# Performance work log

Hardware: AMD Instinct MI355X
Metric: run time of the kernel (lower is better)

Reference implementation:

```python
import jax, jax.numpy as jnp
import numpy as np

B, S, D, H = 2, 2048, 1024, 16
DK = D // H  # 64


def setup_inputs() -> dict:
    key = jax.random.key(0)
    ks = jax.random.split(key, 9)
    s = 0.02
    return {
        "embeddings": jax.random.normal(ks[0], (B, S, D), jnp.float32),
        "Wq": jax.random.normal(ks[1], (H, D, DK), jnp.float32) * s,
        "bq": jax.random.normal(ks[2], (H, DK), jnp.float32) * s,
        "Wk": jax.random.normal(ks[3], (H, D, DK), jnp.float32) * s,
        "bk": jax.random.normal(ks[4], (H, DK), jnp.float32) * s,
        "Wv": jax.random.normal(ks[5], (H, D, DK), jnp.float32) * s,
        "bv": jax.random.normal(ks[6], (H, DK), jnp.float32) * s,
        "Wo": jax.random.normal(ks[7], (D, D), jnp.float32) * s,
        "bo": jax.random.normal(ks[8], (D,), jnp.float32) * s,
    }


def reference(embeddings, Wq, bq, Wk, bk, Wv, bv, Wo, bo):
    b, s, d = embeddings.shape
    dk = Wq.shape[-1]
    # batched per-head projections: [b,s,d] x [h,d,k] -> [b,h,s,k]
    q = jnp.einsum('bsd,hdk->bhsk', embeddings, Wq) + bq[None, :, None, :]
    k = jnp.einsum('bsd,hdk->bhsk', embeddings, Wk) + bk[None, :, None, :]
    v = jnp.einsum('bsd,hdk->bhsk', embeddings, Wv) + bv[None, :, None, :]
    scores = jnp.einsum('bhqk,bhsk->bhqs', q, k) / jnp.sqrt(jnp.float32(dk))
    causal_mask = jnp.triu(jnp.ones((s, s), dtype=bool), k=1)  # True above diagonal
    scores = jnp.where(causal_mask, jnp.float32(-1e9), scores)
    weights = jax.nn.softmax(scores, axis=-1)
    ctx = jnp.einsum('bhqs,bhsk->bhqk', weights, v)
    concat = ctx.transpose(0, 2, 1, 3).reshape(b, s, d)  # head-major concat, matches torch.cat
    return concat @ Wo + bo
```

## Files before the change

### kernel.cpp

```cpp
#include <hip/hip_runtime.h>
#include <hip/hip_bf16.h>

typedef unsigned short u16;
typedef unsigned int u32;
typedef __bf16 bf16x8 __attribute__((ext_vector_type(8)));
typedef float f32x4 __attribute__((ext_vector_type(4)));

#define AS1 __attribute__((address_space(1)))
#define AS3 __attribute__((address_space(3)))

#define NB 2
#define NS 2048
#define ND 1024
#define NH 16
#define NK 64

__device__ __forceinline__ u16 f2bf(float f) {
  u32 u = __builtin_bit_cast(u32, f);
  return (u16)((u + 0x7FFFu + ((u >> 16) & 1u)) >> 16);
}

__device__ __forceinline__ u32 cvt_pk_bf16(float lo, float hi) {
  u32 u;
  asm("v_cvt_pk_bf16_f32 %0, %1, %2" : "=v"(u) : "v"(lo), "v"(hi));
  return u;
}

__device__ __forceinline__ void stage_tile(u16* lds, const u16* __restrict__ src, int rs,
                                           int wid, int lane) {
#pragma unroll
  for (int i = 0; i < 2; ++i) {
    int c = wid * 128 + i * 64 + lane;
    int row = c >> 3;
    int kc = (c & 7) ^ (row & 7);
    __builtin_amdgcn_global_load_lds((const AS1 u32*)(src + row * rs + kc * 8),
                                     (AS3 u32*)(lds + (wid * 128 + i * 64) * 8), 16, 0, 0);
  }
}

__device__ __forceinline__ bf16x8 read_frag(const u16* lds, int row, int ks, int lane) {
  int slot = ((lane >> 4) + ks * 4) ^ (row & 7);
  return *(const bf16x8*)(lds + row * 64 + slot * 8);
}

__global__ __launch_bounds__(256) void convert_kernel(const float* __restrict__ src,
                                                      u16* __restrict__ dst, int n) {
  int i = (blockIdx.x * 256 + threadIdx.x) * 4;
  if (i >= n) return;
  float4 v = *(const float4*)(src + i);
  u32 w0 = cvt_pk_bf16(v.x, v.y);
  u32 w1 = cvt_pk_bf16(v.z, v.w);
  uint2 w; w.x = w0; w.y = w1;
  *(uint2*)(dst + i) = w;
}

__global__ __launch_bounds__(256) void transpose_conv(const float* __restrict__ src,
                                                      u16* __restrict__ dst, int R, int C) {
  __shared__ float tile[32][33];
  size_t base = (size_t)blockIdx.z * R * C;
  src += base;
  dst += base;
  int c0 = blockIdx.x * 32, r0 = blockIdx.y * 32;
  int tx = threadIdx.x, ty = threadIdx.y;
#pragma unroll
  for (int i = 0; i < 4; ++i)
    tile[ty + 8 * i][tx] = src[(size_t)(r0 + ty + 8 * i) * C + c0 + tx];
  __syncthreads();
#pragma unroll
  for (int i = 0; i < 4; ++i)
    dst[(size_t)(c0 + ty + 8 * i) * R + r0 + tx] = f2bf(tile[tx][ty + 8 * i]);
}

__global__ __launch_bounds__(256) void qkv_kernel(
    const u16* __restrict__ emb, const u16* __restrict__ Wqt, const u16* __restrict__ Wkt,
    const u16* __restrict__ Wvt, const float* __restrict__ bq, const float* __restrict__ bk,
    const float* __restrict__ bv, u16* __restrict__ Q, u16* __restrict__ K,
    u16* __restrict__ Vt) {
  __shared__ alignas(16) u16 lds_a[64 * 64];
  __shared__ alignas(16) u16 lds_b[64 * 64];
  int tid = threadIdx.x, lane = tid & 63, wid = tid >> 6;
  int mt = blockIdx.x, h = blockIdx.y, which = blockIdx.z;
  const u16* Wt = (which == 0 ? Wqt : which == 1 ? Wkt : Wvt) + h * (ND * NK);
  const float* bias = (which == 0 ? bq : which == 1 ? bk : bv) + h * NK;
  int m0 = mt * 64;
  int col = lane & 15;
  f32x4 zero4 = {0.f, 0.f, 0.f, 0.f};
  f32x4 acc[4] = {zero4, zero4, zero4, zero4};
  for (int k0 = 0; k0 < ND; k0 += 64) {
    stage_tile(lds_a, emb + m0 * ND + k0, ND, wid, lane);
    stage_tile(lds_b, Wt + k0, ND, wid, lane);
    __syncthreads();
#pragma unroll
    for (int ks = 0; ks < 2; ++ks) {
      bf16x8 a = read_frag(lds_a, wid * 16 + col, ks, lane);
#pragma unroll
      for (int f = 0; f < 4; ++f) {
        bf16x8 b = read_frag(lds_b, f * 16 + col, ks, lane);
        acc[f] = __builtin_amdgcn_mfma_f32_16x16x32_bf16(a, b, acc[f], 0, 0, 0);
      }
    }
    __syncthreads();
  }
  int rbase = m0 + wid * 16 + (lane >> 4) * 4;
#pragma unroll
  for (int f = 0; f < 4; ++f) {
    int n = f * 16 + col;
    float bn = bias[n];
#pragma unroll
    for (int r = 0; r < 4; ++r) {
      int m = rbase + r;
      int b = m >> 11, s = m & (NS - 1);
      float v = acc[f][r] + bn;
      if (which == 0) {
        Q[((b * NH + h) * NS + s) * NK + n] = f2bf(v * 0.18033688f);
      } else if (which == 1) {
        K[((b * NH + h) * NS + s) * NK + n] = f2bf(v);
      } else {
        Vt[((b * NH + h) * NK + n) * NS + s] = f2bf(v);
      }
    }
  }
}

__global__ __launch_bounds__(256) void attn_kernel(const u16* __restrict__ Q,
                                                   const u16* __restrict__ K,
                                                   const u16* __restrict__ Vt,
                                                   u16* __restrict__ ctx) {
  __shared__ alignas(16) u16 lds_k[2][64 * 64];
  __shared__ alignas(16) u16 lds_v[2][64 * 64];
  __shared__ alignas(16) u16 p_lds[4][16 * 72];
  int tid = threadIdx.x, lane = tid & 63, wid = tid >> 6;
  int bh = blockIdx.x;
  int pr = blockIdx.y;
  const u16* Qb = Q + bh * (NS * NK);
  const u16* Kb = K + bh * (NS * NK);
  const u16* Vb = Vt + bh * (NK * NS);
  int col = lane & 15;
  int b = bh >> 4, h = bh & 15;
  f32x4 zero4 = {0.f, 0.f, 0.f, 0.f};
  u16* pw = p_lds[wid];

#pragma unroll 1
  for (int half = 0; half < 2; ++half) {
    int qt = half ? pr : (31 - pr);
    int q0 = qt * 64;
    int qrow_a = q0 + wid * 16 + col;
    bf16x8 qf0 = *(const bf16x8*)(Qb + qrow_a * NK + (lane >> 4) * 8);
    bf16x8 qf1 = *(const bf16x8*)(Qb + qrow_a * NK + 32 + (lane >> 4) * 8);
    f32x4 acc[4] = {zero4, zero4, zero4, zero4};
    float m[4], lp[4];
#pragma unroll
    for (int r = 0; r < 4; ++r) { m[r] = -1e30f; lp[r] = 0.f; }
    int qrow_c = q0 + wid * 16 + (lane >> 4) * 4;
    int nt = qt + 1;

    stage_tile(lds_k[0], Kb, NK, wid, lane);
    stage_tile(lds_v[0], Vb, NS, wid, lane);
    __syncthreads();

    for (int t = 0; t < nt; ++t) {
      int cur = t & 1;
      if (t + 1 < nt) {
        stage_tile(lds_k[cur ^ 1], Kb + (t + 1) * 64 * NK, NK, wid, lane);
        stage_tile(lds_v[cur ^ 1], Vb + (t + 1) * 64, NS, wid, lane);
      }
      const u16* lk = lds_k[cur];
      const u16* lv = lds_v[cur];
      f32x4 sc[4];
#pragma unroll
      for (int f = 0; f < 4; ++f) {
        bf16x8 b0 = read_frag(lk, f * 16 + col, 0, lane);
        sc[f] = __builtin_amdgcn_mfma_f32_16x16x32_bf16(qf0, b0, zero4, 0, 0, 0);
        bf16x8 b1 = read_frag(lk, f * 16 + col, 1, lane);
        sc[f] = __builtin_amdgcn_mfma_f32_16x16x32_bf16(qf1, b1, sc[f], 0, 0, 0);
      }
      if (t == qt) {
#pragma unroll
        for (int f = 0; f < 4; ++f) {
          int kg = t * 64 + f * 16 + col;
#pragma unroll
          for (int r = 0; r < 4; ++r)
            if (kg > qrow_c + r) sc[f][r] = -1e30f;
        }
      }
      float mx[4];
#pragma unroll
      for (int r = 0; r < 4; ++r)
        mx[r] = fmaxf(fmaxf(sc[0][r], sc[1][r]), fmaxf(sc[2][r], sc[3][r]));
#pragma unroll
      for (int off = 1; off < 16; off <<= 1)
#pragma unroll
        for (int r = 0; r < 4; ++r) mx[r] = fmaxf(mx[r], __shfl_xor(mx[r], off));
      bool ok = true;
#pragma unroll
      for (int r = 0; r < 4; ++r) ok = ok && (mx[r] <= m[r] + 8.0f);
      if (!__all(ok)) {
#pragma unroll
        for (int r = 0; r < 4; ++r) {
          float mn = fmaxf(m[r], mx[r]);
          float al = exp2f(m[r] - mn);
          m[r] = mn;
          lp[r] *= al;
#pragma unroll
          for (int f = 0; f < 4; ++f) acc[f][r] *= al;
        }
      }
#pragma unroll
      for (int f = 0; f < 4; ++f)
#pragma unroll
        for (int r = 0; r < 4; ++r) {
          float p = exp2f(sc[f][r] - m[r]);
          sc[f][r] = p;
          lp[r] += p;
        }
#pragma unroll
      for (int f = 0; f < 4; ++f)
#pragma unroll
        for (int rp = 0; rp < 4; rp += 2) {
          u32 u = cvt_pk_bf16(sc[f][rp], sc[f][rp + 1]);
          int row = (lane >> 4) * 4 + rp;
          pw[row * 72 + f * 16 + col] = (u16)u;
          pw[(row + 1) * 72 + f * 16 + col] = (u16)(u >> 16);
        }
#pragma unroll
      for (int ks = 0; ks < 2; ++ks) {
        bf16x8 pa = *(const bf16x8*)(pw + col * 72 + ks * 32 + (lane >> 4) * 8);
#pragma unroll
        for (int f = 0; f < 4; ++f) {
          bf16x8 vb = read_frag(lv, f * 16 + col, ks, lane);
          acc[f] = __builtin_amdgcn_mfma_f32_16x16x32_bf16(pa, vb, acc[f], 0, 0, 0);
        }
      }
      __syncthreads();
    }
#pragma unroll
    for (int off = 1; off < 16; off <<= 1)
#pragma unroll
      for (int r = 0; r < 4; ++r) lp[r] += __shfl_xor(lp[r], off);
#pragma unroll
    for (int r = 0; r < 4; ++r) {
      float inv = 1.0f / lp[r];
      int s = qrow_c + r;
#pragma unroll
      for (int f = 0; f < 4; ++f)
        ctx[(b * NS + s) * ND + h * NK + f * 16 + col] = f2bf(acc[f][r] * inv);
    }
  }
}

__global__ __launch_bounds__(256) void outproj_kernel(const u16* __restrict__ ctx,
                                                      const u16* __restrict__ Wot,
                                                      const float* __restrict__ bo,
                                                      float* __restrict__ out) {
  __shared__ alignas(16) u16 lds_a[64 * 64];
  __shared__ alignas(16) u16 lds_b[64 * 64];
  int tid = threadIdx.x, lane = tid & 63, wid = tid >> 6;
  int m0 = blockIdx.x * 64, n0 = blockIdx.y * 64;
  int col = lane & 15;
  f32x4 zero4 = {0.f, 0.f, 0.f, 0.f};
  f32x4 acc[4] = {zero4, zero4, zero4, zero4};
  for (int k0 = 0; k0 < ND; k0 += 64) {
    stage_tile(lds_a, ctx + m0 * ND + k0, ND, wid, lane);
    stage_tile(lds_b, Wot + n0 * ND + k0, ND, wid, lane);
    __syncthreads();
#pragma unroll
    for (int ks = 0; ks < 2; ++ks) {
      bf16x8 a = read_frag(lds_a, wid * 16 + col, ks, lane);
#pragma unroll
      for (int f = 0; f < 4; ++f) {
        bf16x8 b = read_frag(lds_b, f * 16 + col, ks, lane);
        acc[f] = __builtin_amdgcn_mfma_f32_16x16x32_bf16(a, b, acc[f], 0, 0, 0);
      }
    }
    __syncthreads();
  }
  int rbase = m0 + wid * 16 + (lane >> 4) * 4;
#pragma unroll
  for (int f = 0; f < 4; ++f) {
    int n = n0 + f * 16 + col;
    float bn = bo[n];
#pragma unroll
    for (int r = 0; r < 4; ++r) out[(rbase + r) * ND + n] = acc[f][r] + bn;
  }
}

extern "C" void kernel_launch(void* const* d_in, const int* in_sizes, int n_in,
                              void* d_out, int out_size, void* d_ws, size_t ws_size,
                              hipStream_t stream) {
  (void)in_sizes; (void)n_in; (void)out_size;
  const float* emb = (const float*)d_in[0];
  const float* Wq = (const float*)d_in[1];
  const float* bq = (const float*)d_in[2];
  const float* Wk = (const float*)d_in[3];
  const float* bk = (const float*)d_in[4];
  const float* Wv = (const float*)d_in[5];
  const float* bv = (const float*)d_in[6];
  const float* Wo = (const float*)d_in[7];
  const float* bo = (const float*)d_in[8];
  float* out = (float*)d_out;

  const size_t EMB_N = (size_t)NB * NS * ND;
  const size_t W_N = (size_t)NH * ND * NK;
  const size_t QKV_N = (size_t)NB * NH * NS * NK;
  if (ws_size < (EMB_N + 4 * W_N + 3 * QKV_N) * sizeof(u16)) return;
  u16* ws = (u16*)d_ws;
  u16* emb_bf = ws;
  u16* Wqt = emb_bf + EMB_N;
  u16* Wkt = Wqt + W_N;
  u16* Wvt = Wkt + W_N;
  u16* Wot = Wvt + W_N;
  u16* Qb = Wot + W_N;
  u16* Kb = Qb + QKV_N;
  u16* Vtb = Kb + QKV_N;
  u16* ctxb = emb_bf;

  convert_kernel<<<dim3((int)(EMB_N / 4 / 256)), dim3(256), 0, stream>>>(emb, emb_bf,
                                                                         (int)EMB_N);
  dim3 tb(32, 8);
  transpose_conv<<<dim3(2, 32, 16), tb, 0, stream>>>(Wq, Wqt, ND, NK);
  transpose_conv<<<dim3(2, 32, 16), tb, 0, stream>>>(Wk, Wkt, ND, NK);
  transpose_conv<<<dim3(2, 32, 16), tb, 0, stream>>>(Wv, Wvt, ND, NK);
  transpose_conv<<<dim3(32, 32, 1), tb, 0, stream>>>(Wo, Wot, ND, ND);
  qkv_kernel<<<dim3(64, 16, 3), dim3(256), 0, stream>>>(emb_bf, Wqt, Wkt, Wvt, bq, bk, bv,
                                                        Qb, Kb, Vtb);
  attn_kernel<<<dim3(32, 16), dim3(256), 0, stream>>>(Qb, Kb, Vtb, ctxb);
  outproj_kernel<<<dim3(64, 16), dim3(256), 0, stream>>>(ctxb, Wot, bo, out);
}
```

Baseline: 139.6 us.

## Rewrite attention with 32x32x16 MFMA, transposed S tile, 128-row query blocks

Reworks the flash-attention kernel to compute S^T with 32x32x16 bf16 MFMAs, so each lane owns one query row. The P fragments can then be packed in registers and fed straight into the PV MFMA, with no LDS round-trip for P. Each block now handles a 128-row query tile, four waves of 32 rows, with a balanced qt mapping instead of paired halves. It adds s_setprio around the MFMA bursts and occupancy 2, and skips tiles past a wave's causal limit while still joining the barriers. The tradeoffs are higher register pressure from the f32x16 accumulators, a small LDS slab to broadcast the rescale factors, and idle waves on the diagonal tiles.

```diff
diff --git a/kernel.cpp b/kernel.cpp
--- a/kernel.cpp
+++ b/kernel.cpp
@@ -5,6 +5,7 @@
 typedef unsigned int u32;
 typedef __bf16 bf16x8 __attribute__((ext_vector_type(8)));
 typedef float f32x4 __attribute__((ext_vector_type(4)));
+typedef float f32x16 __attribute__((ext_vector_type(16)));
 
 #define AS1 __attribute__((address_space(1)))
 #define AS3 __attribute__((address_space(3)))
@@ -36,6 +37,23 @@
     __builtin_amdgcn_global_load_lds((const AS1 u32*)(src + row * rs + kc * 8),
                                      (AS3 u32*)(lds + (wid * 128 + i * 64) * 8), 16, 0, 0);
   }
+}
+
+__device__ __forceinline__ bf16x8 read_slot(const u16* lds, int row, int slot) {
+  return *(const bf16x8*)(lds + row * 64 + (slot ^ (row & 7)) * 8);
+}
+
+__device__ __forceinline__ uint2 ld8(const u16* lds, int row, int col) {
+  int slot = (col >> 3) ^ (row & 7);
+  return *(const uint2*)(lds + row * 64 + slot * 8 + (col & 7));
+}
+
+__device__ __forceinline__ bf16x8 read_vfrag(const u16* lds, int row, int ks, int hi) {
+  int c0 = ks * 16 + 4 * hi;
+  uint2 a = ld8(lds, row, c0);
+  uint2 b = ld8(lds, row, c0 + 8);
+  uint4 q; q.x = a.x; q.y = a.y; q.z = b.x; q.w = b.y;
+  return __builtin_bit_cast(bf16x8, q);
 }
 
 __device__ __forceinline__ bf16x8 read_frag(const u16* lds, int row, int ks, int lane) {
@@ -122,129 +140,141 @@
   }
 }
 
-__global__ __launch_bounds__(256) void attn_kernel(const u16* __restrict__ Q,
-                                                   const u16* __restrict__ K,
-                                                   const u16* __restrict__ Vt,
-                                                   u16* __restrict__ ctx) {
+__global__ __launch_bounds__(256, 2) void attn_kernel(const u16* __restrict__ Q,
+                                                      const u16* __restrict__ K,
+                                                      const u16* __restrict__ Vt,
+                                                      u16* __restrict__ ctx) {
   __shared__ alignas(16) u16 lds_k[2][64 * 64];
   __shared__ alignas(16) u16 lds_v[2][64 * 64];
-  __shared__ alignas(16) u16 p_lds[4][16 * 72];
-  int tid = threadIdx.x, lane = tid & 63, wid = tid >> 6;
+  __shared__ float slab[4][32];
+  int tid = threadIdx.x, lane = tid & 63, w = tid >> 6;
+  int hi = lane >> 5, ln = lane & 31;
   int bh = blockIdx.x;
-  int pr = blockIdx.y;
+  int y = blockIdx.y;
+  int qt = (y < 8) ? (15 - y) : (y - 8);
   const u16* Qb = Q + bh * (NS * NK);
   const u16* Kb = K + bh * (NS * NK);
   const u16* Vb = Vt + bh * (NK * NS);
-  int col = lane & 15;
-  int b = bh >> 4, h = bh & 15;
-  f32x4 zero4 = {0.f, 0.f, 0.f, 0.f};
-  u16* pw = p_lds[wid];
-
-#pragma unroll 1
-  for (int half = 0; half < 2; ++half) {
-    int qt = half ? pr : (31 - pr);
-    int q0 = qt * 64;
-    int qrow_a = q0 + wid * 16 + col;
-    bf16x8 qf0 = *(const bf16x8*)(Qb + qrow_a * NK + (lane >> 4) * 8);
-    bf16x8 qf1 = *(const bf16x8*)(Qb + qrow_a * NK + 32 + (lane >> 4) * 8);
-    f32x4 acc[4] = {zero4, zero4, zero4, zero4};
-    float m[4], lp[4];
-#pragma unroll
-    for (int r = 0; r < 4; ++r) { m[r] = -1e30f; lp[r] = 0.f; }
-    int qrow_c = q0 + wid * 16 + (lane >> 4) * 4;
-    int nt = qt + 1;
-
-    stage_tile(lds_k[0], Kb, NK, wid, lane);
-    stage_tile(lds_v[0], Vb, NS, wid, lane);
-    __syncthreads();
-
-    for (int t = 0; t < nt; ++t) {
-      int cur = t & 1;
-      if (t + 1 < nt) {
-        stage_tile(lds_k[cur ^ 1], Kb + (t + 1) * 64 * NK, NK, wid, lane);
-        stage_tile(lds_v[cur ^ 1], Vb + (t + 1) * 64, NS, wid, lane);
-      }
+  int q0w = qt * 128 + w * 32;
+  int qg = q0w + ln;
+  bf16x8 qf[4];
+#pragma unroll
+  for (int ks = 0; ks < 4; ++ks)
+    qf[ks] = *(const bf16x8*)(Qb + qg * NK + ks * 16 + hi * 8);
+
+  f32x16 acc0, acc1;
+#pragma unroll
+  for (int r = 0; r < 16; ++r) { acc0[r] = 0.f; acc1[r] = 0.f; }
+  float m = -1e30f, lp = 0.f;
+  int nt = 2 * qt + 2;
+  int tmaxw = (q0w + 31) >> 6;
+
+  stage_tile(lds_k[0], Kb, NK, w, lane);
+  stage_tile(lds_v[0], Vb, NS, w, lane);
+  __syncthreads();
+
+  for (int t = 0; t < nt; ++t) {
+    int cur = t & 1;
+    if (t + 1 < nt) {
+      stage_tile(lds_k[cur ^ 1], Kb + (t + 1) * 64 * NK, NK, w, lane);
+      stage_tile(lds_v[cur ^ 1], Vb + (t + 1) * 64, NS, w, lane);
+    }
+    if (t <= tmaxw) {
       const u16* lk = lds_k[cur];
       const u16* lv = lds_v[cur];
-      f32x4 sc[4];
-#pragma unroll
-      for (int f = 0; f < 4; ++f) {
-        bf16x8 b0 = read_frag(lk, f * 16 + col, 0, lane);
-        sc[f] = __builtin_amdgcn_mfma_f32_16x16x32_bf16(qf0, b0, zero4, 0, 0, 0);
-        bf16x8 b1 = read_frag(lk, f * 16 + col, 1, lane);
-        sc[f] = __builtin_amdgcn_mfma_f32_16x16x32_bf16(qf1, b1, sc[f], 0, 0, 0);
-      }
-      if (t == qt) {
-#pragma unroll
-        for (int f = 0; f < 4; ++f) {
-          int kg = t * 64 + f * 16 + col;
-#pragma unroll
-          for (int r = 0; r < 4; ++r)
-            if (kg > qrow_c + r) sc[f][r] = -1e30f;
+      f32x16 sc0, sc1;
+#pragma unroll
+      for (int r = 0; r < 16; ++r) { sc0[r] = 0.f; sc1[r] = 0.f; }
+      __builtin_amdgcn_s_setprio(1);
+#pragma unroll
+      for (int ks = 0; ks < 4; ++ks) {
+        bf16x8 kf0 = read_slot(lk, ln, 2 * ks + hi);
+        sc0 = __builtin_amdgcn_mfma_f32_32x32x16_bf16(kf0, qf[ks], sc0, 0, 0, 0);
+        bf16x8 kf1 = read_slot(lk, 32 + ln, 2 * ks + hi);
+        sc1 = __builtin_amdgcn_mfma_f32_32x32x16_bf16(kf1, qf[ks], sc1, 0, 0, 0);
+      }
+      __builtin_amdgcn_s_setprio(0);
+      if (t == tmaxw) {
+#pragma unroll
+        for (int r = 0; r < 16; ++r) {
+          int kl = t * 64 + (r & 3) + 8 * (r >> 2) + 4 * hi;
+          if (kl > qg) sc0[r] = -1e30f;
+          if (kl + 32 > qg) sc1[r] = -1e30f;
         }
       }
-      float mx[4];
-#pragma unroll
-      for (int r = 0; r < 4; ++r)
-        mx[r] = fmaxf(fmaxf(sc[0][r], sc[1][r]), fmaxf(sc[2][r], sc[3][r]));
-#pragma unroll
-      for (int off = 1; off < 16; off <<= 1)
-#pragma unroll
-        for (int r = 0; r < 4; ++r) mx[r] = fmaxf(mx[r], __shfl_xor(mx[r], off));
-      bool ok = true;
-#pragma unroll
-      for (int r = 0; r < 4; ++r) ok = ok && (mx[r] <= m[r] + 8.0f);
-      if (!__all(ok)) {
-#pragma unroll
-        for (int r = 0; r < 4; ++r) {
-          float mn = fmaxf(m[r], mx[r]);
-          float al = exp2f(m[r] - mn);
-          m[r] = mn;
-          lp[r] *= al;
-#pragma unroll
-          for (int f = 0; f < 4; ++f) acc[f][r] *= al;
-        }
-      }
-#pragma unroll
-      for (int f = 0; f < 4; ++f)
-#pragma unroll
-        for (int r = 0; r < 4; ++r) {
-          float p = exp2f(sc[f][r] - m[r]);
-          sc[f][r] = p;
-          lp[r] += p;
-        }
-#pragma unroll
-      for (int f = 0; f < 4; ++f)
-#pragma unroll
-        for (int rp = 0; rp < 4; rp += 2) {
-          u32 u = cvt_pk_bf16(sc[f][rp], sc[f][rp + 1]);
-          int row = (lane >> 4) * 4 + rp;
-          pw[row * 72 + f * 16 + col] = (u16)u;
-          pw[(row + 1) * 72 + f * 16 + col] = (u16)(u >> 16);
-        }
-#pragma unroll
-      for (int ks = 0; ks < 2; ++ks) {
-        bf16x8 pa = *(const bf16x8*)(pw + col * 72 + ks * 32 + (lane >> 4) * 8);
-#pragma unroll
-        for (int f = 0; f < 4; ++f) {
-          bf16x8 vb = read_frag(lv, f * 16 + col, ks, lane);
-          acc[f] = __builtin_amdgcn_mfma_f32_16x16x32_bf16(pa, vb, acc[f], 0, 0, 0);
-        }
-      }
-      __syncthreads();
-    }
-#pragma unroll
-    for (int off = 1; off < 16; off <<= 1)
-#pragma unroll
-      for (int r = 0; r < 4; ++r) lp[r] += __shfl_xor(lp[r], off);
-#pragma unroll
-    for (int r = 0; r < 4; ++r) {
-      float inv = 1.0f / lp[r];
-      int s = qrow_c + r;
-#pragma unroll
-      for (int f = 0; f < 4; ++f)
-        ctx[(b * NS + s) * ND + h * NK + f * 16 + col] = f2bf(acc[f][r] * inv);
-    }
+      float mt_[16];
+#pragma unroll
+      for (int i = 0; i < 16; ++i) mt_[i] = fmaxf(sc0[i], sc1[i]);
+#pragma unroll
+      for (int s = 8; s > 0; s >>= 1)
+#pragma unroll
+        for (int i = 0; i < s; ++i) mt_[i] = fmaxf(mt_[i], mt_[i + s]);
+      float mx = mt_[0];
+      mx = fmaxf(mx, __shfl_xor(mx, 32));
+      if (__any(mx > m + 8.0f)) {
+        float mn = fmaxf(m, mx);
+        float al = exp2f(m - mn);
+        m = mn;
+        lp *= al;
+        if (!hi) slab[w][ln] = al;
+        float av[16];
+#pragma unroll
+        for (int r = 0; r < 16; ++r) av[r] = slab[w][(r & 3) + 8 * (r >> 2) + 4 * hi];
+#pragma unroll
+        for (int r = 0; r < 16; ++r) { acc0[r] *= av[r]; acc1[r] *= av[r]; }
+      }
+      float ps[4] = {0.f, 0.f, 0.f, 0.f};
+#pragma unroll
+      for (int r = 0; r < 16; ++r) {
+        float p = exp2f(sc0[r] - m);
+        sc0[r] = p;
+        ps[r & 3] += p;
+      }
+#pragma unroll
+      for (int r = 0; r < 16; ++r) {
+        float p = exp2f(sc1[r] - m);
+        sc1[r] = p;
+        ps[r & 3] += p;
+      }
+      lp += (ps[0] + ps[1]) + (ps[2] + ps[3]);
+      u32 wd[8];
+      bf16x8 pa[4];
+#pragma unroll
+      for (int i = 0; i < 8; ++i) wd[i] = cvt_pk_bf16(sc0[2 * i], sc0[2 * i + 1]);
+      { uint4 q4; q4.x = wd[0]; q4.y = wd[1]; q4.z = wd[2]; q4.w = wd[3];
+        pa[0] = __builtin_bit_cast(bf16x8, q4);
+        q4.x = wd[4]; q4.y = wd[5]; q4.z = wd[6]; q4.w = wd[7];
+        pa[1] = __builtin_bit_cast(bf16x8, q4); }
+#pragma unroll
+      for (int i = 0; i < 8; ++i) wd[i] = cvt_pk_bf16(sc1[2 * i], sc1[2 * i + 1]);
+      { uint4 q4; q4.x = wd[0]; q4.y = wd[1]; q4.z = wd[2]; q4.w = wd[3];
+        pa[2] = __builtin_bit_cast(bf16x8, q4);
+        q4.x = wd[4]; q4.y = wd[5]; q4.z = wd[6]; q4.w = wd[7];
+        pa[3] = __builtin_bit_cast(bf16x8, q4); }
+      __builtin_amdgcn_s_setprio(1);
+#pragma unroll
+      for (int ks = 0; ks < 4; ++ks) {
+        bf16x8 vf0 = read_vfrag(lv, ln, ks, hi);
+        acc0 = __builtin_amdgcn_mfma_f32_32x32x16_bf16(pa[ks], vf0, acc0, 0, 0, 0);
+        bf16x8 vf1 = read_vfrag(lv, 32 + ln, ks, hi);
+        acc1 = __builtin_amdgcn_mfma_f32_32x32x16_bf16(pa[ks], vf1, acc1, 0, 0, 0);
+      }
+      __builtin_amdgcn_s_setprio(0);
+    }
+    __syncthreads();
+  }
+  lp += __shfl_xor(lp, 32);
+  if (!hi) slab[w][ln] = 1.0f / lp;
+  float iv[16];
+#pragma unroll
+  for (int r = 0; r < 16; ++r) iv[r] = slab[w][(r & 3) + 8 * (r >> 2) + 4 * hi];
+  int b = bh >> 4, h = bh & 15;
+#pragma unroll
+  for (int r = 0; r < 16; ++r) {
+    int qq = q0w + (r & 3) + 8 * (r >> 2) + 4 * hi;
+    size_t base = (size_t)(b * NS + qq) * ND + h * NK + ln;
+    ctx[base] = f2bf(acc0[r] * iv[r]);
+    ctx[base + 32] = f2bf(acc1[r] * iv[r]);
   }
 }
 
```

Result: no change. 138.4 us (-0.9%).
